# Kernel tuning notes

Measured on AMD Instinct MI355X. Metric: run time of the kernel, lower is better.

The kernel has to match this reference:

```python
import jax, jax.numpy as jnp
import numpy as np
from jax import lax

DN = ('NHWC', 'HWIO', 'NHWC')

def _conv(a, w):
    return lax.conv_general_dilated(a, w, (1, 1), 'SAME', dimension_numbers=DN)

def _hard_sigmoid(z):
    return jnp.clip(0.2 * z + 0.5, 0.0, 1.0)


def setup_inputs() -> dict:
    key = jax.random.key(0)
    ks = jax.random.split(key, 4)
    B, T, H, W, C, F, K = 2, 16, 64, 64, 64, 64, 3
    x = jax.random.normal(ks[0], (B, T, H, W, C), dtype=jnp.float32)
    Wx = jax.random.normal(ks[1], (K, K, C, 4 * F), dtype=jnp.float32) * (2.0 / (K * K * C)) ** 0.5
    Wh = jax.random.normal(ks[2], (K, K, F, 4 * F), dtype=jnp.float32) * (2.0 / (K * K * F)) ** 0.5
    b = jax.random.normal(ks[3], (4 * F,), dtype=jnp.float32) * 0.01
    gamma = jnp.ones((F,), dtype=jnp.float32)
    beta = jnp.zeros((F,), dtype=jnp.float32)
    moving_mean = jnp.zeros((F,), dtype=jnp.float32)
    moving_var = jnp.ones((F,), dtype=jnp.float32)
    return {"x": x, "Wx": Wx, "Wh": Wh, "b": b, "gamma": gamma,
            "beta": beta, "moving_mean": moving_mean, "moving_var": moving_var}


def reference(x, Wx, Wh, b, gamma, beta, moving_mean, moving_var):
    B, T, H, W, C = x.shape
    F = Wh.shape[2]
    # Precompute the input-to-gate convolutions for all timesteps in one big conv.
    xg = _conv(x.reshape(B * T, H, W, C), Wx) + b          # (B*T, H, W, 4F)
    xg = xg.reshape(B, T, H, W, 4 * F).transpose(1, 0, 2, 3, 4)  # (T, B, H, W, 4F)

    h0 = jnp.zeros((B, H, W, F), dtype=x.dtype)
    c0 = jnp.zeros((B, H, W, F), dtype=x.dtype)

    def step(carry, xt):
        h, c = carry
        z = xt + _conv(h, Wh)                               # (B, H, W, 4F)
        zi, zf, zg, zo = jnp.split(z, 4, axis=-1)           # Keras gate order: i, f, c, o
        i = _hard_sigmoid(zi)
        f = _hard_sigmoid(zf)
        g = jnp.tanh(zg)
        o = _hard_sigmoid(zo)
        c_new = f * c + i * g
        h_new = o * jnp.tanh(c_new)
        return (h_new, c_new), h_new

    _, hs = lax.scan(step, (h0, c0), xg)                    # (T, B, H, W, F)
    out = hs.transpose(1, 0, 2, 3, 4)                       # (B, T, H, W, F)

    # BatchNormalization in inference mode (training=False), eps=1e-3 (Keras default)
    eps = 1e-3
    inv = gamma * lax.rsqrt(moving_var + eps)
    out = out * inv + (beta - moving_mean * inv)
    return out
```

## Files before the change

### kernel.cpp

```cpp
#include <hip/hip_runtime.h>
#include <cstddef>

typedef __attribute__((ext_vector_type(8))) _Float16 half8;
typedef __attribute__((ext_vector_type(4))) float f32x4;
typedef __attribute__((ext_vector_type(4))) unsigned short us4;

#define TT 16
#define APAD 72
#define A_TILE (3*34*APAD)
#define CHUNK  8192
#define NB     6
#define PF     5
#define XNB    4
#define XPF    3

__device__ __forceinline__ unsigned short f2h(float f) {
    return __builtin_bit_cast(unsigned short, (_Float16)f);
}
__device__ __forceinline__ float h2f(unsigned short u) {
    return (float)__builtin_bit_cast(_Float16, u);
}
__device__ __forceinline__ float hsig(float z) {
    return fminf(fmaxf(0.2f * z + 0.5f, 0.f), 1.f);
}

__global__ __launch_bounds__(256) void prep_kernel(
    const float* __restrict__ Wx, const float* __restrict__ Wh,
    const float* __restrict__ gamma, const float* __restrict__ beta,
    const float* __restrict__ mean, const float* __restrict__ var,
    unsigned short* __restrict__ Wc, float* __restrict__ bn)
{
    if (blockIdx.x == 1152) {
        if (threadIdx.x < 64) {
            const int c = threadIdx.x;
            const float inv = gamma[c] * rsqrtf(var[c] + 1e-3f);
            bn[c] = inv;
            bn[64 + c] = beta[c] - mean[c] * inv;
        }
        return;
    }
    const int i = blockIdx.x * 256 + threadIdx.x;
    const int j  = i & 7;
    const int n  = (i >> 3) & 255;
    const int kg = (i >> 11) & 3;
    const int s  = i >> 13;
    const int sub = s % 18;
    const float* W = (s >= 18) ? Wh : Wx;
    const int k5 = sub * 32 + kg * 8 + j;
    const int c = k5 & 63, q = k5 >> 6;
    const int kx = q % 3, ky = q / 3;
    Wc[i] = f2h(W[(size_t)((ky * 3 + kx) * 64 + c) * 256 + n]);
}

#define BLOAD(slot, ci) {                                                     \
    const unsigned short* _p = Wc + (size_t)(ci) * CHUNK + boff;              \
    bp[slot][0] = *(const half8*)_p;                                          \
    bp[slot][1] = *(const half8*)(_p + 128);                                  \
}

template<int C0, int CLAST, int AOFF>
__device__ __forceinline__ void conv_pass18(
    const unsigned short* __restrict__ Wc, const int boff,
    half8 (&bp)[NB][2],
    const unsigned short* abase,
    f32x4 acc[2][2])
{
    #pragma unroll
    for (int sub = 0; sub < 18; ++sub) {
        const int ci = C0 + sub;
        if (ci + PF <= CLAST) BLOAD((ci + PF) % NB, ci + PF)

        const int ky = sub / 6, kx = (sub / 2) % 3, cb = sub & 1;
        const half8 b0 = bp[ci % NB][0];
        const half8 b1 = bp[ci % NB][1];
        const unsigned short* at = abase + AOFF + (ky * 34 + kx) * APAD + cb * 32;
        const half8 a0 = *(const half8*)(at);
        const half8 a1 = *(const half8*)(at + 16 * APAD);
        acc[0][0] = __builtin_amdgcn_mfma_f32_16x16x32_f16(a0, b0, acc[0][0], 0, 0, 0);
        acc[0][1] = __builtin_amdgcn_mfma_f32_16x16x32_f16(a0, b1, acc[0][1], 0, 0, 0);
        acc[1][0] = __builtin_amdgcn_mfma_f32_16x16x32_f16(a1, b0, acc[1][0], 0, 0, 0);
        acc[1][1] = __builtin_amdgcn_mfma_f32_16x16x32_f16(a1, b1, acc[1][1], 0, 0, 0);
    }
}

__global__ __launch_bounds__(512) void xconv_kernel(
    const float* __restrict__ x,
    const unsigned short* __restrict__ Wc,
    const float* __restrict__ bias,
    unsigned short* __restrict__ xg)
{
    const int bid0 = blockIdx.x;
    const int bid = (bid0 & 7) * 256 + (bid0 >> 3);
    const int y = bid & 63;
    const int t = (bid >> 6) & 15;
    const int n = bid >> 10;
    const int tid = threadIdx.x, lane = tid & 63, w = tid >> 6;
    const int p0 = lane & 15, g = lane >> 4;

    __shared__ __align__(16) unsigned short smem[3 * 66 * APAD];

    const int boff = g * 2048 + (w * 32 + p0) * 8;

    half8 bp[XNB][2];
    #pragma unroll
    for (int sc = 0; sc < XPF; ++sc) BLOAD(sc, sc)

    const float* __restrict__ xt = x + (size_t)(n * TT + t) * 4096 * 64;
    for (int idx = tid; idx < 3 * 66 * 8; idx += 512) {
        const int cg  = idx & 7;
        const int col = (idx >> 3) % 66;
        const int r   = (idx >> 3) / 66;
        const int gy = y + r - 1;
        const int gx = col - 1;
        const bool ok = ((unsigned)gy < 64u) && ((unsigned)gx < 64u);
        float4 v0 = make_float4(0.f, 0.f, 0.f, 0.f), v1 = v0;
        if (ok) {
            const float* p = xt + (size_t)(gy * 64 + gx) * 64 + cg * 8;
            v0 = *(const float4*)p;
            v1 = *(const float4*)(p + 4);
        }
        __align__(16) unsigned short os[8];
        os[0] = f2h(v0.x); os[1] = f2h(v0.y); os[2] = f2h(v0.z); os[3] = f2h(v0.w);
        os[4] = f2h(v1.x); os[5] = f2h(v1.y); os[6] = f2h(v1.z); os[7] = f2h(v1.w);
        *(uint4*)&smem[(r * 66 + col) * APAD + cg * 8] = *(const uint4*)os;
    }
    __syncthreads();

    const unsigned short* abase = smem + p0 * APAD + g * 8;

    f32x4 acc[4][2] = {};
    #pragma unroll
    for (int sub = 0; sub < 18; ++sub) {
        if (sub + XPF < 18) BLOAD((sub + XPF) % XNB, sub + XPF)

        const int ky = sub / 6, kx = (sub / 2) % 3, cb = sub & 1;
        const half8 b0 = bp[sub % XNB][0];
        const half8 b1 = bp[sub % XNB][1];
        #pragma unroll
        for (int cq = 0; cq < 4; ++cq) {
            const half8 a = *(const half8*)(abase
                + (ky * 66 + cq * 16 + kx) * APAD + cb * 32);
            acc[cq][0] = __builtin_amdgcn_mfma_f32_16x16x32_f16(a, b0, acc[cq][0], 0, 0, 0);
            acc[cq][1] = __builtin_amdgcn_mfma_f32_16x16x32_f16(a, b1, acc[cq][1], 0, 0, 0);
        }
    }

    const float bv0 = bias[w * 32 + p0];
    const float bv1 = bias[w * 32 + 16 + p0];
    #pragma unroll
    for (int xh2 = 0; xh2 < 2; ++xh2) {
        unsigned short os[16];
        #pragma unroll
        for (int mfc = 0; mfc < 2; ++mfc)
            #pragma unroll
            for (int nf = 0; nf < 2; ++nf)
                #pragma unroll
                for (int j = 0; j < 4; ++j)
                    os[mfc * 8 + nf * 4 + j] =
                        f2h(acc[xh2 * 2 + mfc][nf][j] + (nf ? bv1 : bv0));
        const size_t vi = ((((size_t)(n * TT + t) * 64 + y) * 2 + xh2) * 8 + w) * 64 + lane;
        unsigned short* dst = xg + vi * 16;
        *(uint4*)dst       = *(uint4*)&os[0];
        *(uint4*)(dst + 8) = *(uint4*)&os[8];
    }
}

template<int FUSED>
__global__ __launch_bounds__(512) void convstep_kernel(
    const float* __restrict__ x,
    const unsigned short* __restrict__ hb,
    const unsigned short* __restrict__ Wc,
    const float* __restrict__ bias,
    const unsigned short* __restrict__ xg,
    float* __restrict__ cbuf,
    unsigned short* __restrict__ ho,
    const float* __restrict__ bn,
    float* __restrict__ out,
    const int t)
{
    const int bid0 = blockIdx.x;
    const int bid = (bid0 & 7) * 32 + (bid0 >> 3);
    const int xh = bid & 1;
    const int y  = (bid >> 1) & 63;
    const int n  = bid >> 7;
    const int tid = threadIdx.x;
    const int lane = tid & 63;
    const int w = tid >> 6;
    const int p0 = lane & 15;
    const int g  = lane >> 4;

    constexpr int SMEM_SHORTS = FUSED ? (2 * A_TILE) : 17408;
    __shared__ __align__(16) unsigned short smem[SMEM_SHORTS];

    const int boff = g * 2048 + (w * 32 + p0) * 8;

    unsigned short xs[16];
    if (!FUSED) {
        const size_t vi = ((((size_t)(n * TT + t) * 64 + y) * 2 + xh) * 8 + w) * 64 + lane;
        const uint4* xp = (const uint4*)(xg + vi * 16);
        *(uint4*)&xs[0] = xp[0];
        *(uint4*)&xs[8] = xp[1];
    }

    constexpr int C0 = FUSED ? 0 : 18;
    half8 bp[NB][2];
    #pragma unroll
    for (int sc = 0; sc < PF; ++sc) BLOAD((C0 + sc) % NB, C0 + sc)

    constexpr int NTILE = FUSED ? 2 : 1;
    const float* __restrict__ xt = x + (size_t)(n * TT + t) * 4096 * 64;
    const size_t hbase = (size_t)n * 4096 * 64;
    for (int idx = tid; idx < NTILE * 3 * 34 * 8; idx += 512) {
        const int cg  = idx & 7;
        const int col = (idx >> 3) % 34;
        const int i3  = (idx >> 3) / 34;
        const int r   = i3 % 3;
        const int src = i3 / 3;
        const int gy = y + r - 1;
        const int gx = xh * 32 + col - 1;
        const bool ok = ((unsigned)gy < 64u) && ((unsigned)gx < 64u);
        const int ebase = (r * 34 + col) * APAD + cg * 8;
        if (FUSED && src == 0) {
            float4 v0 = make_float4(0.f, 0.f, 0.f, 0.f), v1 = v0;
            if (ok) {
                const float* p = xt + (size_t)(gy * 64 + gx) * 64 + cg * 8;
                v0 = *(const float4*)p;
                v1 = *(const float4*)(p + 4);
            }
            __align__(16) unsigned short os[8];
            os[0] = f2h(v0.x); os[1] = f2h(v0.y); os[2] = f2h(v0.z); os[3] = f2h(v0.w);
            os[4] = f2h(v1.x); os[5] = f2h(v1.y); os[6] = f2h(v1.z); os[7] = f2h(v1.w);
            *(uint4*)&smem[ebase] = *(const uint4*)os;
        } else {
            uint4 v = make_uint4(0u, 0u, 0u, 0u);
            if (ok) v = *(const uint4*)(hb + hbase + (size_t)(gy * 64 + gx) * 64 + cg * 8);
            *(uint4*)&smem[(FUSED ? A_TILE : 0) + ebase] = v;
        }
    }
    __syncthreads();

    const unsigned short* abase = smem + p0 * APAD + g * 8;

    f32x4 acc[2][2] = {};
    if (FUSED) {
        conv_pass18<0, 35, 0>(Wc, boff, bp, abase, acc);
        conv_pass18<18, 35, A_TILE>(Wc, boff, bp, abase, acc);
    } else {
        conv_pass18<18, 35, 0>(Wc, boff, bp, abase, acc);
    }

    __syncthreads();
    float* gbuf = (float*)smem;
    const int gate = w >> 1;
    const int chalf = (w & 1) * 32;

    float bv[2];
    bv[0] = bias[w * 32 + p0];
    bv[1] = bias[w * 32 + 16 + p0];

    #pragma unroll
    for (int mf = 0; mf < 2; ++mf)
        #pragma unroll
        for (int nf = 0; nf < 2; ++nf)
            #pragma unroll
            for (int j = 0; j < 4; ++j) {
                float v = acc[mf][nf][j] + (FUSED ? bv[nf] : h2f(xs[mf * 8 + nf * 4 + j]));
                v = (gate == 2) ? tanhf(v) : hsig(v);
                const int px = mf * 16 + g * 4 + j;
                gbuf[(gate * 32 + px) * 68 + chalf + nf * 16 + p0] = v;
            }
    __syncthreads();

    const int p  = tid >> 4;
    const int c4 = (tid & 15) * 4;
    const float4 iv = *(const float4*)&gbuf[(0 * 32 + p) * 68 + c4];
    const float4 fv = *(const float4*)&gbuf[(1 * 32 + p) * 68 + c4];
    const float4 gv = *(const float4*)&gbuf[(2 * 32 + p) * 68 + c4];
    const float4 ov = *(const float4*)&gbuf[(3 * 32 + p) * 68 + c4];
    const size_t gpix = (size_t)((n * 64 + y) * 64 + xh * 32 + p);
    const size_t sb = gpix * 64 + c4;
    const float4 cold = *(const float4*)&cbuf[sb];
    const float4 scv  = *(const float4*)&bn[c4];
    const float4 shv  = *(const float4*)&bn[64 + c4];

    const float ivv[4] = {iv.x, iv.y, iv.z, iv.w};
    const float fvv[4] = {fv.x, fv.y, fv.z, fv.w};
    const float gvv[4] = {gv.x, gv.y, gv.z, gv.w};
    const float ovv[4] = {ov.x, ov.y, ov.z, ov.w};
    const float cov[4] = {cold.x, cold.y, cold.z, cold.w};
    const float scc[4] = {scv.x, scv.y, scv.z, scv.w};
    const float shh[4] = {shv.x, shv.y, shv.z, shv.w};

    float cnew[4], obuf[4];
    us4 hh;
    unsigned short* hhp = (unsigned short*)&hh;
    #pragma unroll
    for (int j = 0; j < 4; ++j) {
        const float cn = fvv[j] * cov[j] + ivv[j] * gvv[j];
        const float hn = ovv[j] * tanhf(cn);
        cnew[j] = cn;
        hhp[j] = f2h(hn);
        obuf[j] = hn * scc[j] + shh[j];
    }
    *(float4*)&cbuf[sb] = *(float4*)&cnew[0];
    *(us4*)&ho[sb]      = hh;
    const size_t ob = ((size_t)((n * TT + t) * 4096 + y * 64 + xh * 32 + p)) * 64 + c4;
    *(float4*)&out[ob] = *(float4*)&obuf[0];
}

extern "C" void kernel_launch(void* const* d_in, const int* in_sizes, int n_in,
                              void* d_out, int out_size, void* d_ws, size_t ws_size,
                              hipStream_t stream) {
    const float* x     = (const float*)d_in[0];
    const float* Wx    = (const float*)d_in[1];
    const float* Wh    = (const float*)d_in[2];
    const float* b     = (const float*)d_in[3];
    const float* gamma = (const float*)d_in[4];
    const float* beta  = (const float*)d_in[5];
    const float* mean  = (const float*)d_in[6];
    const float* var   = (const float*)d_in[7];
    float* out = (float*)d_out;
    char* ws = (char*)d_ws;

    unsigned short* Wc   = (unsigned short*)(ws);
    float*          bn   = (float*)(ws + 589824);
    unsigned short* hA   = (unsigned short*)(ws + 590336);
    float*          cbuf = (float*)(ws + 1638912);
    unsigned short* hB   = (unsigned short*)(ws + 3736064);
    unsigned short* xg   = (unsigned short*)(ws + 4784640);
    const size_t NEED = 4784640ull + 67108864ull;

    hipMemsetAsync(ws + 590336, 0, 3145728, stream);
    prep_kernel<<<1153, 256, 0, stream>>>(Wx, Wh, gamma, beta, mean, var, Wc, bn);

    if (ws_size >= NEED) {
        xconv_kernel<<<2048, 512, 0, stream>>>(x, Wc, b, xg);
        for (int t = 0; t < TT; ++t) {
            const bool even = (t & 1) == 0;
            convstep_kernel<0><<<256, 512, 0, stream>>>(
                x, even ? hA : hB, Wc, b, xg, cbuf, even ? hB : hA, bn, out, t);
        }
    } else {
        for (int t = 0; t < TT; ++t) {
            const bool even = (t & 1) == 0;
            convstep_kernel<1><<<256, 512, 0, stream>>>(
                x, even ? hA : hB, Wc, b, xg, cbuf, even ? hB : hA, bn, out, t);
        }
    }
}
```

Before: 200.8 us.

## Swizzle LDS tiles and remap convstep waves to gate-per-accumulator layout

Applies a modulo-9 slot swizzle to the LDS input tiles in xconv and the new recurrent step kernel, aiming to reduce bank conflicts on the A-fragment reads. The recurrent step kernel is rewritten so each wave owns 16 pixels by 16 channels across all four gates. The i/f/g/o activations and the cell/hidden update can then run in registers, with no LDS gate-buffer round trip and no extra barriers. The cost is more B-fragment registers per wave and scalar (non-vectorised) global stores for cbuf, h and out.

New measurement: 214.9 us. 7.1% more time.

```diff
diff --git a/kernel.cpp b/kernel.cpp
--- a/kernel.cpp
+++ b/kernel.cpp
@@ -13,6 +13,8 @@
 #define PF     5
 #define XNB    4
 #define XPF    3
+#define SNB    4
+#define SPF    3
 
 __device__ __forceinline__ unsigned short f2h(float f) {
     return __builtin_bit_cast(unsigned short, (_Float16)f);
@@ -108,8 +110,9 @@
     const float* __restrict__ xt = x + (size_t)(n * TT + t) * 4096 * 64;
     for (int idx = tid; idx < 3 * 66 * 8; idx += 512) {
         const int cg  = idx & 7;
-        const int col = (idx >> 3) % 66;
-        const int r   = (idx >> 3) / 66;
+        const int COL = idx >> 3;
+        const int col = COL % 66;
+        const int r   = COL / 66;
         const int gy = y + r - 1;
         const int gx = col - 1;
         const bool ok = ((unsigned)gy < 64u) && ((unsigned)gx < 64u);
@@ -122,11 +125,10 @@
         __align__(16) unsigned short os[8];
         os[0] = f2h(v0.x); os[1] = f2h(v0.y); os[2] = f2h(v0.z); os[3] = f2h(v0.w);
         os[4] = f2h(v1.x); os[5] = f2h(v1.y); os[6] = f2h(v1.z); os[7] = f2h(v1.w);
-        *(uint4*)&smem[(r * 66 + col) * APAD + cg * 8] = *(const uint4*)os;
+        const int slot = (cg + COL) % 9;
+        *(uint4*)&smem[COL * APAD + slot * 8] = *(const uint4*)os;
     }
     __syncthreads();
-
-    const unsigned short* abase = smem + p0 * APAD + g * 8;
 
     f32x4 acc[4][2] = {};
     #pragma unroll
@@ -136,10 +138,12 @@
         const int ky = sub / 6, kx = (sub / 2) % 3, cb = sub & 1;
         const half8 b0 = bp[sub % XNB][0];
         const half8 b1 = bp[sub % XNB][1];
+        const int u = g + 4 * cb;
         #pragma unroll
         for (int cq = 0; cq < 4; ++cq) {
-            const half8 a = *(const half8*)(abase
-                + (ky * 66 + cq * 16 + kx) * APAD + cb * 32);
+            const int COLa = ky * 66 + cq * 16 + kx + p0;
+            const int slot = (u + COLa) % 9;
+            const half8 a = *(const half8*)(smem + COLa * APAD + slot * 8);
             acc[cq][0] = __builtin_amdgcn_mfma_f32_16x16x32_f16(a, b0, acc[cq][0], 0, 0, 0);
             acc[cq][1] = __builtin_amdgcn_mfma_f32_16x16x32_f16(a, b1, acc[cq][1], 0, 0, 0);
         }
@@ -165,13 +169,115 @@
     }
 }
 
-template<int FUSED>
-__global__ __launch_bounds__(512) void convstep_kernel(
+__global__ __launch_bounds__(512) void convstep2_kernel(
+    const unsigned short* __restrict__ hb,
+    const unsigned short* __restrict__ Wc,
+    const unsigned short* __restrict__ xg,
+    float* __restrict__ cbuf,
+    unsigned short* __restrict__ ho,
+    const float* __restrict__ bn,
+    float* __restrict__ out,
+    const int t)
+{
+    const int bid0 = blockIdx.x;
+    const int bid = (bid0 & 7) * 32 + (bid0 >> 3);
+    const int xh = bid & 1;
+    const int y  = (bid >> 1) & 63;
+    const int n  = bid >> 7;
+    const int tid = threadIdx.x;
+    const int lane = tid & 63;
+    const int w = tid >> 6;
+    const int ph = w >> 2;
+    const int cb = w & 3;
+    const int p0 = lane & 15;
+    const int g  = lane >> 4;
+
+    __shared__ __align__(16) unsigned short smem[A_TILE];
+
+    const int cbh = cb >> 1, cbl = cb & 1;
+    us4 xs4[4];
+    #pragma unroll
+    for (int gate = 0; gate < 4; ++gate) {
+        const size_t vi = ((((size_t)(n * TT + t) * 64 + y) * 2 + xh) * 8
+                           + (gate * 2 + cbh)) * 64 + lane;
+        xs4[gate] = *(const us4*)(xg + vi * 16 + ph * 8 + cbl * 4);
+    }
+
+    const unsigned short* wbase = Wc + (size_t)18 * CHUNK + g * 2048 + cb * 128 + p0 * 8;
+    half8 bp[SNB][4];
+    #pragma unroll
+    for (int sc = 0; sc < SPF; ++sc) {
+        const unsigned short* _p = wbase + (size_t)sc * CHUNK;
+        bp[sc][0] = *(const half8*)(_p);
+        bp[sc][1] = *(const half8*)(_p + 512);
+        bp[sc][2] = *(const half8*)(_p + 1024);
+        bp[sc][3] = *(const half8*)(_p + 1536);
+    }
+
+    const size_t hbase = (size_t)n * 4096 * 64;
+    for (int idx = tid; idx < 3 * 34 * 8; idx += 512) {
+        const int cg  = idx & 7;
+        const int COL = idx >> 3;
+        const int col = COL % 34;
+        const int r   = COL / 34;
+        const int gy = y + r - 1;
+        const int gx = xh * 32 + col - 1;
+        uint4 v = make_uint4(0u, 0u, 0u, 0u);
+        if (((unsigned)gy < 64u) && ((unsigned)gx < 64u))
+            v = *(const uint4*)(hb + hbase + (size_t)(gy * 64 + gx) * 64 + cg * 8);
+        const int slot = (cg + COL) % 9;
+        *(uint4*)&smem[COL * APAD + slot * 8] = v;
+    }
+    __syncthreads();
+
+    f32x4 acc[4] = {};
+    #pragma unroll
+    for (int sub = 0; sub < 18; ++sub) {
+        if (sub + SPF < 18) {
+            const int slot = (sub + SPF) % SNB;
+            const unsigned short* _p = wbase + (size_t)(sub + SPF) * CHUNK;
+            bp[slot][0] = *(const half8*)(_p);
+            bp[slot][1] = *(const half8*)(_p + 512);
+            bp[slot][2] = *(const half8*)(_p + 1024);
+            bp[slot][3] = *(const half8*)(_p + 1536);
+        }
+        const int ky = sub / 6, kx = (sub / 2) % 3, cbs = sub & 1;
+        const int COLa = ky * 34 + ph * 16 + p0 + kx;
+        const int slot = (g + 4 * cbs + COLa) % 9;
+        const half8 a = *(const half8*)(smem + COLa * APAD + slot * 8);
+        const int bs = sub % SNB;
+        acc[0] = __builtin_amdgcn_mfma_f32_16x16x32_f16(a, bp[bs][0], acc[0], 0, 0, 0);
+        acc[1] = __builtin_amdgcn_mfma_f32_16x16x32_f16(a, bp[bs][1], acc[1], 0, 0, 0);
+        acc[2] = __builtin_amdgcn_mfma_f32_16x16x32_f16(a, bp[bs][2], acc[2], 0, 0, 0);
+        acc[3] = __builtin_amdgcn_mfma_f32_16x16x32_f16(a, bp[bs][3], acc[3], 0, 0, 0);
+    }
+
+    const int c64 = cb * 16 + p0;
+    const float scs = bn[c64];
+    const float shs = bn[64 + c64];
+    #pragma unroll
+    for (int j = 0; j < 4; ++j) {
+        const int px = ph * 16 + g * 4 + j;
+        const float ig = hsig(acc[0][j] + h2f(xs4[0][j]));
+        const float fg = hsig(acc[1][j] + h2f(xs4[1][j]));
+        const float gg = tanhf(acc[2][j] + h2f(xs4[2][j]));
+        const float og = hsig(acc[3][j] + h2f(xs4[3][j]));
+        const size_t sb = ((size_t)((n * 64 + y) * 64 + xh * 32 + px)) * 64 + c64;
+        const float cold = cbuf[sb];
+        const float cn = fg * cold + ig * gg;
+        const float hn = og * tanhf(cn);
+        cbuf[sb] = cn;
+        ho[sb] = f2h(hn);
+        out[((size_t)((n * TT + t) * 4096 + y * 64 + xh * 32 + px)) * 64 + c64]
+            = hn * scs + shs;
+    }
+}
+
+__global__ __launch_bounds__(512) void convstep_fused(
     const float* __restrict__ x,
     const unsigned short* __restrict__ hb,
     const unsigned short* __restrict__ Wc,
     const float* __restrict__ bias,
-    const unsigned short* __restrict__ xg,
     float* __restrict__ cbuf,
     unsigned short* __restrict__ ho,
     const float* __restrict__ bn,
@@ -189,28 +295,16 @@
     const int p0 = lane & 15;
     const int g  = lane >> 4;
 
-    constexpr int SMEM_SHORTS = FUSED ? (2 * A_TILE) : 17408;
-    __shared__ __align__(16) unsigned short smem[SMEM_SHORTS];
+    __shared__ __align__(16) unsigned short smem[2 * A_TILE + 2720];
 
     const int boff = g * 2048 + (w * 32 + p0) * 8;
-
-    unsigned short xs[16];
-    if (!FUSED) {
-        const size_t vi = ((((size_t)(n * TT + t) * 64 + y) * 2 + xh) * 8 + w) * 64 + lane;
-        const uint4* xp = (const uint4*)(xg + vi * 16);
-        *(uint4*)&xs[0] = xp[0];
-        *(uint4*)&xs[8] = xp[1];
-    }
-
-    constexpr int C0 = FUSED ? 0 : 18;
     half8 bp[NB][2];
     #pragma unroll
-    for (int sc = 0; sc < PF; ++sc) BLOAD((C0 + sc) % NB, C0 + sc)
-
-    constexpr int NTILE = FUSED ? 2 : 1;
+    for (int sc = 0; sc < PF; ++sc) BLOAD(sc, sc)
+
     const float* __restrict__ xt = x + (size_t)(n * TT + t) * 4096 * 64;
     const size_t hbase = (size_t)n * 4096 * 64;
-    for (int idx = tid; idx < NTILE * 3 * 34 * 8; idx += 512) {
+    for (int idx = tid; idx < 2 * 3 * 34 * 8; idx += 512) {
         const int cg  = idx & 7;
         const int col = (idx >> 3) % 34;
         const int i3  = (idx >> 3) / 34;
@@ -220,7 +314,7 @@
         const int gx = xh * 32 + col - 1;
         const bool ok = ((unsigned)gy < 64u) && ((unsigned)gx < 64u);
         const int ebase = (r * 34 + col) * APAD + cg * 8;
-        if (FUSED && src == 0) {
+        if (src == 0) {
             float4 v0 = make_float4(0.f, 0.f, 0.f, 0.f), v1 = v0;
             if (ok) {
                 const float* p = xt + (size_t)(gy * 64 + gx) * 64 + cg * 8;
@@ -234,26 +328,20 @@
         } else {
             uint4 v = make_uint4(0u, 0u, 0u, 0u);
             if (ok) v = *(const uint4*)(hb + hbase + (size_t)(gy * 64 + gx) * 64 + cg * 8);
-            *(uint4*)&smem[(FUSED ? A_TILE : 0) + ebase] = v;
+            *(uint4*)&smem[A_TILE + ebase] = v;
         }
     }
     __syncthreads();
 
     const unsigned short* abase = smem + p0 * APAD + g * 8;
-
     f32x4 acc[2][2] = {};
-    if (FUSED) {
-        conv_pass18<0, 35, 0>(Wc, boff, bp, abase, acc);
-        conv_pass18<18, 35, A_TILE>(Wc, boff, bp, abase, acc);
-    } else {
-        conv_pass18<18, 35, 0>(Wc, boff, bp, abase, acc);
-    }
+    conv_pass18<0, 35, 0>(Wc, boff, bp, abase, acc);
+    conv_pass18<18, 35, A_TILE>(Wc, boff, bp, abase, acc);
 
     __syncthreads();
     float* gbuf = (float*)smem;
     const int gate = w >> 1;
     const int chalf = (w & 1) * 32;
-
     float bv[2];
     bv[0] = bias[w * 32 + p0];
     bv[1] = bias[w * 32 + 16 + p0];
@@ -264,7 +352,7 @@
         for (int nf = 0; nf < 2; ++nf)
             #pragma unroll
             for (int j = 0; j < 4; ++j) {
-                float v = acc[mf][nf][j] + (FUSED ? bv[nf] : h2f(xs[mf * 8 + nf * 4 + j]));
+                float v = acc[mf][nf][j] + bv[nf];
                 v = (gate == 2) ? tanhf(v) : hsig(v);
                 const int px = mf * 16 + g * 4 + j;
                 gbuf[(gate * 32 + px) * 68 + chalf + nf * 16 + p0] = v;
@@ -277,8 +365,7 @@
     const float4 fv = *(const float4*)&gbuf[(1 * 32 + p) * 68 + c4];
     const float4 gv = *(const float4*)&gbuf[(2 * 32 + p) * 68 + c4];
     const float4 ov = *(const float4*)&gbuf[(3 * 32 + p) * 68 + c4];
-    const size_t gpix = (size_t)((n * 64 + y) * 64 + xh * 32 + p);
-    const size_t sb = gpix * 64 + c4;
+    const size_t sb = ((size_t)((n * 64 + y) * 64 + xh * 32 + p)) * 64 + c4;
     const float4 cold = *(const float4*)&cbuf[sb];
     const float4 scv  = *(const float4*)&bn[c4];
     const float4 shv  = *(const float4*)&bn[64 + c4];
@@ -337,14 +424,14 @@
         xconv_kernel<<<2048, 512, 0, stream>>>(x, Wc, b, xg);
         for (int t = 0; t < TT; ++t) {
             const bool even = (t & 1) == 0;
-            convstep_kernel<0><<<256, 512, 0, stream>>>(
-                x, even ? hA : hB, Wc, b, xg, cbuf, even ? hB : hA, bn, out, t);
+            convstep2_kernel<<<256, 512, 0, stream>>>(
+                even ? hA : hB, Wc, xg, cbuf, even ? hB : hA, bn, out, t);
         }
     } else {
         for (int t = 0; t < TT; ++t) {
             const bool even = (t & 1) == 0;
-            convstep_kernel<1><<<256, 512, 0, stream>>>(
-                x, even ? hA : hB, Wc, b, xg, cbuf, even ? hB : hA, bn, out, t);
-        }
-    }
-}
+            convstep_fused<<<256, 512, 0, stream>>>(
+                x, even ? hA : hB, Wc, b, cbuf, even ? hB : hA, bn, out, t);
+        }
+    }
+}
```

## Add 16-pixel-wide recurrent step kernel doubling block count

Applied to the files above, without the earlier changes.

Adds a specialized recurrent step kernel that processes 16 output pixels per block instead of 32, launching 512 blocks rather than 256 per timestep. It is meant to fill more compute units on the GPU, since 256 blocks underuse the device during the serial per-timestep recurrence. The trade-off is a larger halo fraction per block (18 of 16 columns loaded) and the weight fragments being loaded by twice as many blocks.

Result: slower. 218.9 us, median of 2 (+9.0%).

```diff
diff --git a/kernel.cpp b/kernel.cpp
--- a/kernel.cpp
+++ b/kernel.cpp
@@ -163,6 +163,106 @@
         *(uint4*)dst       = *(uint4*)&os[0];
         *(uint4*)(dst + 8) = *(uint4*)&os[8];
     }
+}
+
+__global__ __launch_bounds__(512) void convstep16_kernel(
+    const unsigned short* __restrict__ hb,
+    const unsigned short* __restrict__ Wc,
+    const unsigned short* __restrict__ xg,
+    float* __restrict__ cbuf,
+    unsigned short* __restrict__ ho,
+    const float* __restrict__ bn,
+    float* __restrict__ out,
+    const int t)
+{
+    const int bid0 = blockIdx.x;
+    const int bid = (bid0 & 7) * 64 + (bid0 >> 3);
+    const int xq = bid & 3;
+    const int y  = (bid >> 2) & 63;
+    const int n  = bid >> 8;
+    const int tid = threadIdx.x;
+    const int lane = tid & 63;
+    const int w = tid >> 6;
+    const int p0 = lane & 15;
+    const int g  = lane >> 4;
+
+    __shared__ __align__(16) unsigned short smem[8704];
+
+    unsigned short xs[8];
+    {
+        const size_t vi = ((((size_t)(n * TT + t) * 64 + y) * 2 + (xq >> 1)) * 8 + w) * 64 + lane;
+        *(uint4*)&xs[0] = *(const uint4*)(xg + vi * 16 + (xq & 1) * 8);
+    }
+
+    const int boff = g * 2048 + (w * 32 + p0) * 8;
+    half8 bp[NB][2];
+    #pragma unroll
+    for (int sc = 0; sc < PF; ++sc) BLOAD((18 + sc) % NB, 18 + sc)
+
+    const size_t hbase = (size_t)n * 4096 * 64;
+    for (int idx = tid; idx < 3 * 18 * 8; idx += 512) {
+        const int cg  = idx & 7;
+        const int col = (idx >> 3) % 18;
+        const int r   = (idx >> 3) / 18;
+        const int gy = y + r - 1;
+        const int gx = xq * 16 + col - 1;
+        uint4 v = make_uint4(0u, 0u, 0u, 0u);
+        if (((unsigned)gy < 64u) && ((unsigned)gx < 64u))
+            v = *(const uint4*)(hb + hbase + (size_t)(gy * 64 + gx) * 64 + cg * 8);
+        *(uint4*)&smem[(r * 18 + col) * APAD + cg * 8] = v;
+    }
+    __syncthreads();
+
+    const unsigned short* abase = smem + p0 * APAD + g * 8;
+    f32x4 acc[2] = {};
+    #pragma unroll
+    for (int sub = 0; sub < 18; ++sub) {
+        const int ci = 18 + sub;
+        if (ci + PF <= 35) BLOAD((ci + PF) % NB, ci + PF)
+
+        const int ky = sub / 6, kx = (sub / 2) % 3, cb = sub & 1;
+        const half8 b0 = bp[ci % NB][0];
+        const half8 b1 = bp[ci % NB][1];
+        const half8 a = *(const half8*)(abase + (ky * 18 + kx) * APAD + cb * 32);
+        acc[0] = __builtin_amdgcn_mfma_f32_16x16x32_f16(a, b0, acc[0], 0, 0, 0);
+        acc[1] = __builtin_amdgcn_mfma_f32_16x16x32_f16(a, b1, acc[1], 0, 0, 0);
+    }
+
+    __syncthreads();
+    float* gbuf = (float*)smem;
+    const int gate = w >> 1;
+    const int chalf = (w & 1) * 32;
+    #pragma unroll
+    for (int nf = 0; nf < 2; ++nf)
+        #pragma unroll
+        for (int j = 0; j < 4; ++j) {
+            float v = acc[nf][j] + h2f(xs[nf * 4 + j]);
+            v = (gate == 2) ? tanhf(v) : hsig(v);
+            const int px = g * 4 + j;
+            gbuf[(gate * 16 + px) * 68 + chalf + nf * 16 + p0] = v;
+        }
+    __syncthreads();
+
+    const int p  = tid >> 5;
+    const int c2 = (tid & 31) * 2;
+    const float2 iv = *(const float2*)&gbuf[(0 * 16 + p) * 68 + c2];
+    const float2 fv = *(const float2*)&gbuf[(1 * 16 + p) * 68 + c2];
+    const float2 gv = *(const float2*)&gbuf[(2 * 16 + p) * 68 + c2];
+    const float2 ov = *(const float2*)&gbuf[(3 * 16 + p) * 68 + c2];
+    const size_t sb = ((size_t)((n * 64 + y) * 64 + xq * 16 + p)) * 64 + c2;
+    const float2 cold = *(const float2*)&cbuf[sb];
+    const float2 scv  = *(const float2*)&bn[c2];
+    const float2 shv  = *(const float2*)&bn[64 + c2];
+
+    const float cn0 = fv.x * cold.x + iv.x * gv.x;
+    const float cn1 = fv.y * cold.y + iv.y * gv.y;
+    const float hn0 = ov.x * tanhf(cn0);
+    const float hn1 = ov.y * tanhf(cn1);
+    *(float2*)&cbuf[sb] = make_float2(cn0, cn1);
+    const unsigned int hh = (unsigned int)f2h(hn0) | ((unsigned int)f2h(hn1) << 16);
+    *(unsigned int*)&ho[sb] = hh;
+    const size_t ob = ((size_t)((n * TT + t) * 4096 + y * 64 + xq * 16 + p)) * 64 + c2;
+    *(float2*)&out[ob] = make_float2(hn0 * scv.x + shv.x, hn1 * scv.y + shv.y);
 }
 
 template<int FUSED>
@@ -277,8 +377,7 @@
     const float4 fv = *(const float4*)&gbuf[(1 * 32 + p) * 68 + c4];
     const float4 gv = *(const float4*)&gbuf[(2 * 32 + p) * 68 + c4];
     const float4 ov = *(const float4*)&gbuf[(3 * 32 + p) * 68 + c4];
-    const size_t gpix = (size_t)((n * 64 + y) * 64 + xh * 32 + p);
-    const size_t sb = gpix * 64 + c4;
+    const size_t sb = ((size_t)((n * 64 + y) * 64 + xh * 32 + p)) * 64 + c4;
     const float4 cold = *(const float4*)&cbuf[sb];
     const float4 scv  = *(const float4*)&bn[c4];
     const float4 shv  = *(const float4*)&bn[64 + c4];
@@ -337,8 +436,8 @@
         xconv_kernel<<<2048, 512, 0, stream>>>(x, Wc, b, xg);
         for (int t = 0; t < TT; ++t) {
             const bool even = (t & 1) == 0;
-            convstep_kernel<0><<<256, 512, 0, stream>>>(
-                x, even ? hA : hB, Wc, b, xg, cbuf, even ? hB : hA, bn, out, t);
+            convstep16_kernel<<<512, 512, 0, stream>>>(
+                even ? hA : hB, Wc, xg, cbuf, even ? hB : hA, bn, out, t);
         }
     } else {
         for (int t = 0; t < TT; ++t) {
```
